# Kernel optimization log

Measured on AMD Instinct MI355X. Metric: run time of the kernel, lower is better.

## Reference

```python
import jax, jax.numpy as jnp
import numpy as np

VOCAB, EMB, ENC = 100000, 256, 256
N_INTENTS, N_SLOTS, LEN_INTENT = 64, 128, 64
B, S = 64, 128


def setup_inputs() -> dict:
    key = jax.random.key(0)
    ks = jax.random.split(key, 8)
    sc = 0.02
    return {
        "token_ids": jax.random.randint(ks[0], (B, S), 0, VOCAB),
        "all_intents": jax.random.randint(ks[1], (B,), 0, N_INTENTS),
        "emb_table": jax.random.normal(ks[2], (VOCAB, EMB), jnp.float32) * sc,
        "doc_enc_W": jax.random.normal(ks[3], (EMB, ENC), jnp.float32) * sc,
        "doc_enc_b": jnp.zeros((ENC,), jnp.float32),
        "slot_enc_W": jax.random.normal(ks[4], (EMB, ENC), jnp.float32) * sc,
        "slot_enc_b": jnp.zeros((ENC,), jnp.float32),
        "doc_dec_W": jax.random.normal(ks[5], (ENC, N_INTENTS), jnp.float32) * sc,
        "doc_dec_b": jnp.zeros((N_INTENTS,), jnp.float32),
        "slot_dec_W": jax.random.normal(ks[6], (ENC + LEN_INTENT, N_SLOTS), jnp.float32) * sc,
        "slot_dec_b": jnp.zeros((N_SLOTS,), jnp.float32),
    }


def reference(token_ids, all_intents, emb_table, doc_enc_W, doc_enc_b,
              slot_enc_W, slot_enc_b, doc_dec_W, doc_dec_b,
              slot_dec_W, slot_dec_b):
    # word embedding lookup: [B, S, EMB] (memory-bound gather)
    emb = emb_table[token_ids]
    # doc encoder: pool sentence then project (batched stand-in for the
    # per-sentence python loop in the original encode())
    sent = jnp.mean(emb, axis=1)                                    # [B, EMB]
    sent_enc = jax.nn.relu(sent @ doc_enc_W + doc_enc_b)            # [B, ENC]
    # intent logits (doc_decoder applied per sentence)
    intent_batch = sent_enc @ doc_dec_W + doc_dec_b                 # [B, N_INTENTS]
    # slot encoder: per-word projection (batched stand-in for per-word loop)
    word_enc = jax.nn.relu(jnp.einsum('bse,eh->bsh', emb, slot_enc_W) + slot_enc_b)
    # use_intent: one-hot of given intent appended to every word encoding
    add_feats = jax.nn.one_hot(all_intents, LEN_INTENT, dtype=word_enc.dtype)  # [B, LEN_INTENT]
    add_feats = jnp.broadcast_to(add_feats[:, None, :], (B, S, LEN_INTENT))
    slot_in = jnp.concatenate([word_enc, add_feats], axis=-1)       # [B, S, ENC+LEN_INTENT]
    slots = jnp.einsum('bsh,ho->bso', slot_in, slot_dec_W) + slot_dec_b
    slots_batch = slots.reshape(B * S, N_SLOTS)  # torch.cat along dim 0 over words
    return intent_batch, slots_batch
```

## Files before the change

kernel.cpp:

```cpp
#include <hip/hip_runtime.h>
#include <hip/hip_bf16.h>

typedef __attribute__((ext_vector_type(8))) short bf16x8;
typedef __attribute__((ext_vector_type(4))) float f32x4;

#define BATCH 64
#define SEQ   128
#define EMB   256
#define ENC   256
#define NIN   64
#define NSL   128

static __device__ __forceinline__ bf16x8 cvt8(const float4 lo, const float4 hi) {
    union { bf16x8 v; __hip_bfloat16 h[8]; } u;
    u.h[0] = __float2bfloat16(lo.x); u.h[1] = __float2bfloat16(lo.y);
    u.h[2] = __float2bfloat16(lo.z); u.h[3] = __float2bfloat16(lo.w);
    u.h[4] = __float2bfloat16(hi.x); u.h[5] = __float2bfloat16(hi.y);
    u.h[6] = __float2bfloat16(hi.z); u.h[7] = __float2bfloat16(hi.w);
    return u.v;
}

__global__ __launch_bounds__(256) void prep_doc_kernel(
    const int*   __restrict__ token_ids,
    const float* __restrict__ emb_table,
    const float* __restrict__ doc_enc_W,
    const float* __restrict__ doc_enc_b,
    const float* __restrict__ doc_dec_W,
    const float* __restrict__ doc_dec_b,
    const float* __restrict__ slot_enc_W,
    const float* __restrict__ slot_dec_W,
    __hip_bfloat16* __restrict__ W1T,
    __hip_bfloat16* __restrict__ W2aT,
    float* __restrict__ out_intent)
{
    __shared__ __align__(16) float red[4][256];
    __shared__ float sent[ENC];
    __shared__ float senc[ENC];
    const int blk = blockIdx.x;
    const int t   = threadIdx.x;

    if (blk < 256) {
        const int idx = blk * 256 + t;
        const int k = idx >> 8;
        const int n = idx & 255;
        W1T[n * 256 + k] = __float2bfloat16(slot_enc_W[idx]);
        if (idx < 256 * 128) {
            const int k2 = idx >> 7;
            const int n2 = idx & 127;
            W2aT[n2 * 256 + k2] = __float2bfloat16(slot_dec_W[idx]);
        }
    } else {
        const int b  = blk - 256;
        const int wv = t >> 6;
        const int ln = t & 63;
        const int* toks = token_ids + b * SEQ;

        float4 acc = make_float4(0.f, 0.f, 0.f, 0.f);
        #pragma unroll 8
        for (int i = 0; i < 32; ++i) {
            const long tok = toks[wv * 32 + i];
            const float4 v = *(const float4*)(emb_table + tok * EMB + ln * 4);
            acc.x += v.x; acc.y += v.y; acc.z += v.z; acc.w += v.w;
        }
        *(float4*)(&red[wv][ln * 4]) = acc;
        __syncthreads();

        sent[t] = (red[0][t] + red[1][t] + red[2][t] + red[3][t]) * (1.0f / 128.0f);
        __syncthreads();

        float a = doc_enc_b[t];
        #pragma unroll 16
        for (int k = 0; k < EMB; ++k)
            a = fmaf(sent[k], doc_enc_W[k * ENC + t], a);
        senc[t] = fmaxf(a, 0.f);
        __syncthreads();

        if (t < NIN) {
            float a2 = doc_dec_b[t];
            #pragma unroll 16
            for (int k = 0; k < ENC; ++k)
                a2 = fmaf(senc[k], doc_dec_W[k * NIN + t], a2);
            out_intent[b * NIN + t] = a2;
        }
    }
}

__global__ __launch_bounds__(256) void slots_kernel(
    const int*   __restrict__ token_ids,
    const int*   __restrict__ all_intents,
    const float* __restrict__ emb_table,
    const __hip_bfloat16* __restrict__ W1T,
    const float* __restrict__ b1,
    const __hip_bfloat16* __restrict__ W2aT,
    const float* __restrict__ W2,
    const float* __restrict__ b2,
    float* __restrict__ out_slots)
{
    __shared__ __align__(16) __hip_bfloat16 lds_we[32 * 264];

    const int blk  = blockIdx.x;
    const int row0 = blk * 32;
    const int wave = threadIdx.x >> 6;
    const int lane = threadIdx.x & 63;
    const int l16  = lane & 15;
    const int quad = lane >> 4;

    f32x4 acc[2][4];
    #pragma unroll
    for (int mt = 0; mt < 2; ++mt)
        #pragma unroll
        for (int nt = 0; nt < 4; ++nt)
            acc[mt][nt] = (f32x4){0.f, 0.f, 0.f, 0.f};

    const long tok0 = token_ids[row0 + l16];
    const long tok1 = token_ids[row0 + 16 + l16];
    const float* arow0 = emb_table + tok0 * EMB + quad * 8;
    const float* arow1 = emb_table + tok1 * EMB + quad * 8;
    const int nbase1 = wave * 64;

    #pragma unroll
    for (int ks = 0; ks < 8; ++ks) {
        const bf16x8 a0 = cvt8(*(const float4*)(arow0 + ks * 32),
                               *(const float4*)(arow0 + ks * 32 + 4));
        const bf16x8 a1 = cvt8(*(const float4*)(arow1 + ks * 32),
                               *(const float4*)(arow1 + ks * 32 + 4));
        #pragma unroll
        for (int nt = 0; nt < 4; ++nt) {
            const bf16x8 bf =
                *(const bf16x8*)(W1T + (nbase1 + nt * 16 + l16) * 256 + ks * 32 + quad * 8);
            acc[0][nt] = __builtin_amdgcn_mfma_f32_16x16x32_bf16(a0, bf, acc[0][nt], 0, 0, 0);
            acc[1][nt] = __builtin_amdgcn_mfma_f32_16x16x32_bf16(a1, bf, acc[1][nt], 0, 0, 0);
        }
    }

    #pragma unroll
    for (int nt = 0; nt < 4; ++nt) {
        const int col = nbase1 + nt * 16 + l16;
        const float bias = b1[col];
        #pragma unroll
        for (int mt = 0; mt < 2; ++mt) {
            #pragma unroll
            for (int r = 0; r < 4; ++r) {
                const int row = mt * 16 + quad * 4 + r;
                lds_we[row * 264 + col] =
                    __float2bfloat16(fmaxf(acc[mt][nt][r] + bias, 0.f));
            }
        }
    }
    __syncthreads();

    f32x4 acc2[2][2];
    #pragma unroll
    for (int mt = 0; mt < 2; ++mt)
        #pragma unroll
        for (int nt = 0; nt < 2; ++nt)
            acc2[mt][nt] = (f32x4){0.f, 0.f, 0.f, 0.f};

    const int nbase2 = wave * 32;
    #pragma unroll
    for (int ks = 0; ks < 8; ++ks) {
        const bf16x8 a0 = *(const bf16x8*)(lds_we + l16 * 264 + ks * 32 + quad * 8);
        const bf16x8 a1 = *(const bf16x8*)(lds_we + (16 + l16) * 264 + ks * 32 + quad * 8);
        #pragma unroll
        for (int nt = 0; nt < 2; ++nt) {
            const bf16x8 bf =
                *(const bf16x8*)(W2aT + (nbase2 + nt * 16 + l16) * 256 + ks * 32 + quad * 8);
            acc2[0][nt] = __builtin_amdgcn_mfma_f32_16x16x32_bf16(a0, bf, acc2[0][nt], 0, 0, 0);
            acc2[1][nt] = __builtin_amdgcn_mfma_f32_16x16x32_bf16(a1, bf, acc2[1][nt], 0, 0, 0);
        }
    }

    const int bidx   = row0 >> 7;
    const int intent = all_intents[bidx];
    const float* hotrow = W2 + (256 + intent) * NSL;

    #pragma unroll
    for (int nt = 0; nt < 2; ++nt) {
        const int col = nbase2 + nt * 16 + l16;
        const float add = b2[col] + hotrow[col];
        #pragma unroll
        for (int mt = 0; mt < 2; ++mt) {
            #pragma unroll
            for (int r = 0; r < 4; ++r) {
                const int row = mt * 16 + quad * 4 + r;
                out_slots[(long)(row0 + row) * NSL + col] = acc2[mt][nt][r] + add;
            }
        }
    }
}

extern "C" void kernel_launch(void* const* d_in, const int* in_sizes, int n_in,
                              void* d_out, int out_size, void* d_ws, size_t ws_size,
                              hipStream_t stream) {
    const int*   token_ids   = (const int*)d_in[0];
    const int*   all_intents = (const int*)d_in[1];
    const float* emb_table   = (const float*)d_in[2];
    const float* doc_enc_W   = (const float*)d_in[3];
    const float* doc_enc_b   = (const float*)d_in[4];
    const float* slot_enc_W  = (const float*)d_in[5];
    const float* slot_enc_b  = (const float*)d_in[6];
    const float* doc_dec_W   = (const float*)d_in[7];
    const float* doc_dec_b   = (const float*)d_in[8];
    const float* slot_dec_W  = (const float*)d_in[9];
    const float* slot_dec_b  = (const float*)d_in[10];

    float*          out  = (float*)d_out;
    __hip_bfloat16* W1T  = (__hip_bfloat16*)d_ws;
    __hip_bfloat16* W2aT = W1T + 256 * 256;

    prep_doc_kernel<<<320, 256, 0, stream>>>(
        token_ids, emb_table, doc_enc_W, doc_enc_b, doc_dec_W, doc_dec_b,
        slot_enc_W, slot_dec_W, W1T, W2aT, out);

    slots_kernel<<<256, 256, 0, stream>>>(
        token_ids, all_intents, emb_table, W1T, slot_enc_b,
        W2aT, slot_dec_W, slot_dec_b, out + BATCH * NIN);
}
```

Measured before the change: 181.4 us.

## Fuse weight prep and slot GEMMs into single kernel with on-the-fly bf16 conversion

```diff
diff --git a/kernel.cpp b/kernel.cpp
--- a/kernel.cpp
+++ b/kernel.cpp
@@ -20,49 +20,140 @@
     return u.v;
 }
 
-__global__ __launch_bounds__(256) void prep_doc_kernel(
+static __device__ __forceinline__ bf16x8 load_bT(const float* __restrict__ W,
+                                                 int ldn, int k0, int n) {
+    union { bf16x8 v; __hip_bfloat16 h[8]; } u;
+    #pragma unroll
+    for (int j = 0; j < 8; ++j)
+        u.h[j] = __float2bfloat16(W[(long)(k0 + j) * ldn + n]);
+    return u.v;
+}
+
+__global__ __launch_bounds__(256) void fused_kernel(
     const int*   __restrict__ token_ids,
+    const int*   __restrict__ all_intents,
     const float* __restrict__ emb_table,
     const float* __restrict__ doc_enc_W,
     const float* __restrict__ doc_enc_b,
+    const float* __restrict__ slot_enc_W,
+    const float* __restrict__ slot_enc_b,
     const float* __restrict__ doc_dec_W,
     const float* __restrict__ doc_dec_b,
-    const float* __restrict__ slot_enc_W,
     const float* __restrict__ slot_dec_W,
-    __hip_bfloat16* __restrict__ W1T,
-    __hip_bfloat16* __restrict__ W2aT,
-    float* __restrict__ out_intent)
+    const float* __restrict__ slot_dec_b,
+    float* __restrict__ out_intent,
+    float* __restrict__ out_slots)
 {
+    __shared__ __align__(16) __hip_bfloat16 lds_we[32 * 264];
     __shared__ __align__(16) float red[4][256];
     __shared__ float sent[ENC];
     __shared__ float senc[ENC];
+
     const int blk = blockIdx.x;
-    const int t   = threadIdx.x;
 
     if (blk < 256) {
-        const int idx = blk * 256 + t;
-        const int k = idx >> 8;
-        const int n = idx & 255;
-        W1T[n * 256 + k] = __float2bfloat16(slot_enc_W[idx]);
-        if (idx < 256 * 128) {
-            const int k2 = idx >> 7;
-            const int n2 = idx & 127;
-            W2aT[n2 * 256 + k2] = __float2bfloat16(slot_dec_W[idx]);
+        const int row0 = blk * 32;
+        const int wave = threadIdx.x >> 6;
+        const int lane = threadIdx.x & 63;
+        const int l16  = lane & 15;
+        const int quad = lane >> 4;
+
+        f32x4 acc[2][4];
+        #pragma unroll
+        for (int mt = 0; mt < 2; ++mt)
+            #pragma unroll
+            for (int nt = 0; nt < 4; ++nt)
+                acc[mt][nt] = (f32x4){0.f, 0.f, 0.f, 0.f};
+
+        const long tok0 = token_ids[row0 + l16];
+        const long tok1 = token_ids[row0 + 16 + l16];
+        const float* arow0 = emb_table + tok0 * EMB + quad * 8;
+        const float* arow1 = emb_table + tok1 * EMB + quad * 8;
+        const int nbase1 = wave * 64;
+
+        #pragma unroll
+        for (int ks = 0; ks < 8; ++ks) {
+            const bf16x8 a0 = cvt8(*(const float4*)(arow0 + ks * 32),
+                                   *(const float4*)(arow0 + ks * 32 + 4));
+            const bf16x8 a1 = cvt8(*(const float4*)(arow1 + ks * 32),
+                                   *(const float4*)(arow1 + ks * 32 + 4));
+            const int k0 = ks * 32 + quad * 8;
+            #pragma unroll
+            for (int nt = 0; nt < 4; ++nt) {
+                const bf16x8 bf = load_bT(slot_enc_W, ENC, k0, nbase1 + nt * 16 + l16);
+                acc[0][nt] = __builtin_amdgcn_mfma_f32_16x16x32_bf16(a0, bf, acc[0][nt], 0, 0, 0);
+                acc[1][nt] = __builtin_amdgcn_mfma_f32_16x16x32_bf16(a1, bf, acc[1][nt], 0, 0, 0);
+            }
+        }
+
+        #pragma unroll
+        for (int nt = 0; nt < 4; ++nt) {
+            const int col = nbase1 + nt * 16 + l16;
+            const float bias = slot_enc_b[col];
+            #pragma unroll
+            for (int mt = 0; mt < 2; ++mt) {
+                #pragma unroll
+                for (int r = 0; r < 4; ++r) {
+                    const int row = mt * 16 + quad * 4 + r;
+                    lds_we[row * 264 + col] =
+                        __float2bfloat16(fmaxf(acc[mt][nt][r] + bias, 0.f));
+                }
+            }
+        }
+        __syncthreads();
+
+        f32x4 acc2[2][2];
+        #pragma unroll
+        for (int mt = 0; mt < 2; ++mt)
+            #pragma unroll
+            for (int nt = 0; nt < 2; ++nt)
+                acc2[mt][nt] = (f32x4){0.f, 0.f, 0.f, 0.f};
+
+        const int nbase2 = wave * 32;
+        #pragma unroll
+        for (int ks = 0; ks < 8; ++ks) {
+            const bf16x8 a0 = *(const bf16x8*)(lds_we + l16 * 264 + ks * 32 + quad * 8);
+            const bf16x8 a1 = *(const bf16x8*)(lds_we + (16 + l16) * 264 + ks * 32 + quad * 8);
+            const int k0 = ks * 32 + quad * 8;
+            #pragma unroll
+            for (int nt = 0; nt < 2; ++nt) {
+                const bf16x8 bf = load_bT(slot_dec_W, NSL, k0, nbase2 + nt * 16 + l16);
+                acc2[0][nt] = __builtin_amdgcn_mfma_f32_16x16x32_bf16(a0, bf, acc2[0][nt], 0, 0, 0);
+                acc2[1][nt] = __builtin_amdgcn_mfma_f32_16x16x32_bf16(a1, bf, acc2[1][nt], 0, 0, 0);
+            }
+        }
+
+        const int intent = all_intents[row0 >> 7];
+        const float* hotrow = slot_dec_W + (long)(256 + intent) * NSL;
+
+        #pragma unroll
+        for (int nt = 0; nt < 2; ++nt) {
+            const int col = nbase2 + nt * 16 + l16;
+            const float add = slot_dec_b[col] + hotrow[col];
+            #pragma unroll
+            for (int mt = 0; mt < 2; ++mt) {
+                #pragma unroll
+                for (int r = 0; r < 4; ++r) {
+                    const int row = mt * 16 + quad * 4 + r;
+                    out_slots[(long)(row0 + row) * NSL + col] = acc2[mt][nt][r] + add;
+                }
+            }
         }
     } else {
         const int b  = blk - 256;
+        const int t  = threadIdx.x;
         const int wv = t >> 6;
         const int ln = t & 63;
         const int* toks = token_ids + b * SEQ;
 
-        float4 acc = make_float4(0.f, 0.f, 0.f, 0.f);
+        float4 accv = make_float4(0.f, 0.f, 0.f, 0.f);
         #pragma unroll 8
         for (int i = 0; i < 32; ++i) {
             const long tok = toks[wv * 32 + i];
             const float4 v = *(const float4*)(emb_table + tok * EMB + ln * 4);
-            acc.x += v.x; acc.y += v.y; acc.z += v.z; acc.w += v.w;
-        }
-        *(float4*)(&red[wv][ln * 4]) = acc;
+            accv.x += v.x; accv.y += v.y; accv.z += v.z; accv.w += v.w;
+        }
+        *(float4*)(&red[wv][ln * 4]) = accv;
         __syncthreads();
 
         sent[t] = (red[0][t] + red[1][t] + red[2][t] + red[3][t]) * (1.0f / 128.0f);
@@ -81,110 +172,6 @@
             for (int k = 0; k < ENC; ++k)
                 a2 = fmaf(senc[k], doc_dec_W[k * NIN + t], a2);
             out_intent[b * NIN + t] = a2;
-        }
-    }
-}
-
-__global__ __launch_bounds__(256) void slots_kernel(
-    const int*   __restrict__ token_ids,
-    const int*   __restrict__ all_intents,
-    const float* __restrict__ emb_table,
-    const __hip_bfloat16* __restrict__ W1T,
-    const float* __restrict__ b1,
-    const __hip_bfloat16* __restrict__ W2aT,
-    const float* __restrict__ W2,
-    const float* __restrict__ b2,
-    float* __restrict__ out_slots)
-{
-    __shared__ __align__(16) __hip_bfloat16 lds_we[32 * 264];
-
-    const int blk  = blockIdx.x;
-    const int row0 = blk * 32;
-    const int wave = threadIdx.x >> 6;
-    const int lane = threadIdx.x & 63;
-    const int l16  = lane & 15;
-    const int quad = lane >> 4;
-
-    f32x4 acc[2][4];
-    #pragma unroll
-    for (int mt = 0; mt < 2; ++mt)
-        #pragma unroll
-        for (int nt = 0; nt < 4; ++nt)
-            acc[mt][nt] = (f32x4){0.f, 0.f, 0.f, 0.f};
-
-    const long tok0 = token_ids[row0 + l16];
-    const long tok1 = token_ids[row0 + 16 + l16];
-    const float* arow0 = emb_table + tok0 * EMB + quad * 8;
-    const float* arow1 = emb_table + tok1 * EMB + quad * 8;
-    const int nbase1 = wave * 64;
-
-    #pragma unroll
-    for (int ks = 0; ks < 8; ++ks) {
-        const bf16x8 a0 = cvt8(*(const float4*)(arow0 + ks * 32),
-                               *(const float4*)(arow0 + ks * 32 + 4));
-        const bf16x8 a1 = cvt8(*(const float4*)(arow1 + ks * 32),
-                               *(const float4*)(arow1 + ks * 32 + 4));
-        #pragma unroll
-        for (int nt = 0; nt < 4; ++nt) {
-            const bf16x8 bf =
-                *(const bf16x8*)(W1T + (nbase1 + nt * 16 + l16) * 256 + ks * 32 + quad * 8);
-            acc[0][nt] = __builtin_amdgcn_mfma_f32_16x16x32_bf16(a0, bf, acc[0][nt], 0, 0, 0);
-            acc[1][nt] = __builtin_amdgcn_mfma_f32_16x16x32_bf16(a1, bf, acc[1][nt], 0, 0, 0);
-        }
-    }
-
-    #pragma unroll
-    for (int nt = 0; nt < 4; ++nt) {
-        const int col = nbase1 + nt * 16 + l16;
-        const float bias = b1[col];
-        #pragma unroll
-        for (int mt = 0; mt < 2; ++mt) {
-            #pragma unroll
-            for (int r = 0; r < 4; ++r) {
-                const int row = mt * 16 + quad * 4 + r;
-                lds_we[row * 264 + col] =
-                    __float2bfloat16(fmaxf(acc[mt][nt][r] + bias, 0.f));
-            }
-        }
-    }
-    __syncthreads();
-
-    f32x4 acc2[2][2];
-    #pragma unroll
-    for (int mt = 0; mt < 2; ++mt)
-        #pragma unroll
-        for (int nt = 0; nt < 2; ++nt)
-            acc2[mt][nt] = (f32x4){0.f, 0.f, 0.f, 0.f};
-
-    const int nbase2 = wave * 32;
-    #pragma unroll
-    for (int ks = 0; ks < 8; ++ks) {
-        const bf16x8 a0 = *(const bf16x8*)(lds_we + l16 * 264 + ks * 32 + quad * 8);
-        const bf16x8 a1 = *(const bf16x8*)(lds_we + (16 + l16) * 264 + ks * 32 + quad * 8);
-        #pragma unroll
-        for (int nt = 0; nt < 2; ++nt) {
-            const bf16x8 bf =
-                *(const bf16x8*)(W2aT + (nbase2 + nt * 16 + l16) * 256 + ks * 32 + quad * 8);
-            acc2[0][nt] = __builtin_amdgcn_mfma_f32_16x16x32_bf16(a0, bf, acc2[0][nt], 0, 0, 0);
-            acc2[1][nt] = __builtin_amdgcn_mfma_f32_16x16x32_bf16(a1, bf, acc2[1][nt], 0, 0, 0);
-        }
-    }
-
-    const int bidx   = row0 >> 7;
-    const int intent = all_intents[bidx];
-    const float* hotrow = W2 + (256 + intent) * NSL;
-
-    #pragma unroll
-    for (int nt = 0; nt < 2; ++nt) {
-        const int col = nbase2 + nt * 16 + l16;
-        const float add = b2[col] + hotrow[col];
-        #pragma unroll
-        for (int mt = 0; mt < 2; ++mt) {
-            #pragma unroll
-            for (int r = 0; r < 4; ++r) {
-                const int row = mt * 16 + quad * 4 + r;
-                out_slots[(long)(row0 + row) * NSL + col] = acc2[mt][nt][r] + add;
-            }
         }
     }
 }
@@ -204,15 +191,10 @@
     const float* slot_dec_W  = (const float*)d_in[9];
     const float* slot_dec_b  = (const float*)d_in[10];
 
-    float*          out  = (float*)d_out;
-    __hip_bfloat16* W1T  = (__hip_bfloat16*)d_ws;
-    __hip_bfloat16* W2aT = W1T + 256 * 256;
-
-    prep_doc_kernel<<<320, 256, 0, stream>>>(
-        token_ids, emb_table, doc_enc_W, doc_enc_b, doc_dec_W, doc_dec_b,
-        slot_enc_W, slot_dec_W, W1T, W2aT, out);
-
-    slots_kernel<<<256, 256, 0, stream>>>(
-        token_ids, all_intents, emb_table, W1T, slot_enc_b,
-        W2aT, slot_dec_W, slot_dec_b, out + BATCH * NIN);
-}
+    float* out = (float*)d_out;
+
+    fused_kernel<<<320, 256, 0, stream>>>(
+        token_ids, all_intents, emb_table, doc_enc_W, doc_enc_b,
+        slot_enc_W, slot_enc_b, doc_dec_W, doc_dec_b, slot_dec_W, slot_dec_b,
+        out, out + BATCH * NIN);
+}
```

New measurement: 171.2 us. -5.6%, faster.
